# Kernel tuning notes

Hardware: AMD Instinct MI355X
Metric: run time of the kernel (lower is better)

Reference implementation:

```python
import jax, jax.numpy as jnp
import numpy as np

DT = 0.01
T, D_IN, D_STATE = 262144, 64, 128

def setup_inputs() -> dict:
    key = jax.random.key(0)
    k1, k2, k3, k4 = jax.random.split(key, 4)
    U = jax.random.normal(k1, (T, D_IN), dtype=jnp.float32)
    A_log = jax.random.normal(k2, (D_STATE,), dtype=jnp.float32) * 0.1 - 1.0
    B = jax.random.normal(k3, (D_STATE, D_IN), dtype=jnp.float32) * 0.1
    C = jax.random.normal(k4, (D_IN, D_STATE), dtype=jnp.float32) * 0.1
    Dm = jnp.zeros((D_IN, D_IN), dtype=jnp.float32)
    h0 = jnp.zeros((D_STATE,), dtype=jnp.float32)
    return {"U": U, "A_log": A_log, "B": B, "C": C, "D": Dm, "h0": h0}

def reference(U, A_log, B, C, D, h0):
    # Discretized diagonal transition: A_disc = exp(A_log * dt)
    A_d = jnp.exp(A_log * DT)  # (d_state,)
    Bu = U @ B.T               # (T, d_state), precompute all input injections
    Du = U @ D.T               # (T, d_input)

    def step(h, bu):
        h_new = A_d * h + bu
        return h_new, h_new

    h_final, H = jax.lax.scan(step, h0, Bu)  # H: (T, d_state)
    Y = H @ C.T + Du                          # (T, d_input)
    return Y, h_final
```

## Files before the change

### kernel.cpp

```cpp
#include <hip/hip_runtime.h>


#define TT   262144
#define DIN  64
#define DS   128
#define DTC  0.01f
#define L    128
#define NG   (TT / L)
#define SEGL 16
#define NSEG (NG / SEGL)

typedef short  s8v  __attribute__((ext_vector_type(8)));
typedef short  s4v  __attribute__((ext_vector_type(4)));
typedef float  f4v  __attribute__((ext_vector_type(4)));

__device__ __forceinline__ unsigned short f2bf(float f) {
    unsigned u = __float_as_uint(f);
    u += 0x7fffu + ((u >> 16) & 1u);
    return (unsigned short)(u >> 16);
}

__device__ __forceinline__ s8v pack8(float4 a, float4 b) {
    union { unsigned short u[8]; s8v v; } r;
    r.u[0] = f2bf(a.x); r.u[1] = f2bf(a.y); r.u[2] = f2bf(a.z); r.u[3] = f2bf(a.w);
    r.u[4] = f2bf(b.x); r.u[5] = f2bf(b.y); r.u[6] = f2bf(b.z); r.u[7] = f2bf(b.w);
    return r.v;
}

__device__ __forceinline__ s4v pack4(float x, float y, float z, float w) {
    union { unsigned short u[4]; s4v v; } r;
    r.u[0] = f2bf(x); r.u[1] = f2bf(y); r.u[2] = f2bf(z); r.u[3] = f2bf(w);
    return r.v;
}

__device__ __forceinline__ int gidx(int NCO, int rtile, int co, int mf) {
    return (((rtile * NCO + co) << 4) + (mf ^ (co & 15))) << 3;
}

__device__ __forceinline__ s8v ldfrag(const unsigned short* S, int NCO,
                                      int rtile, int kt, int q, int m) {
    return *(const s8v*)&S[gidx(NCO, rtile, kt * 4 + q, m)];
}

__device__ __forceinline__ void stage_U(const float* __restrict__ Ug,
                                        unsigned short* __restrict__ sA,
                                        int tid) {
    #pragma unroll
    for (int p = 0; p < 2; ++p) {
        int u  = tid + p * 512;
        int co = u & 7, m = (u >> 3) & 15, mt = u >> 7;
        const float4* gp = (const float4*)(Ug + (mt * 16 + m) * DIN + co * 8);
        *(s8v*)&sA[gidx(8, mt, co, m)] = pack8(gp[0], gp[1]);
    }
}

__device__ __forceinline__ s8v load_bfrag(const float* __restrict__ M,
                                          int row, int k0, int ld) {
    const float4* p = (const float4*)(M + row * ld + k0);
    return pack8(p[0], p[1]);
}

__global__ __launch_bounds__(512, 8) void ssm_k1(
    const float* __restrict__ U, const float* __restrict__ Alog,
    const float* __restrict__ B, float* __restrict__ agg,
    float* __restrict__ segAgg)
{
    __shared__ __align__(16) unsigned short sA[8192];
    const int g    = blockIdx.x;
    const int tid  = threadIdx.x;
    const int lane = tid & 63;
    const int w    = tid >> 6;
    const int q    = lane >> 4, m = lane & 15;
    const int s    = 16 * w + m;

    stage_U(U + (size_t)g * L * DIN, sA, tid);

    s8v Bf[2];
    #pragma unroll
    for (int ks = 0; ks < 2; ++ks)
        Bf[ks] = load_bfrag(B, s, ks * 32 + q * 8, DIN);

    const float cA = Alog[s] * DTC;
    __syncthreads();

    float ainv = __expf(-cA);
    float a16i = __expf(-16.f * cA);
    float wmt  = __expf(cA * (float)(127 - 4 * q));
    float wsum = 0.f;
    #pragma unroll
    for (int mt = 0; mt < 8; ++mt) {
        f4v acc = (f4v){0.f, 0.f, 0.f, 0.f};
        #pragma unroll
        for (int ks = 0; ks < 2; ++ks)
            acc = __builtin_amdgcn_mfma_f32_16x16x32_bf16(
                ldfrag(sA, 8, mt, ks, q, m), Bf[ks], acc, 0, 0, 0);
        float wr = wmt;
        #pragma unroll
        for (int r = 0; r < 4; ++r) {
            wsum = fmaf(wr, acc[r], wsum);
            wr *= ainv;
        }
        wmt *= a16i;
    }
    wsum += __shfl_xor(wsum, 16, 64);
    wsum += __shfl_xor(wsum, 32, 64);

    if (q == 0) {
        agg[(size_t)g * DS + s] = wsum;
        float wgt = __expf(cA * (float)(L * (SEGL - 1 - (g & (SEGL - 1)))));
        atomicAdd(&segAgg[(g >> 4) * DS + s], wsum * wgt);
    }
}

__global__ void ssm_k2(const float* __restrict__ Alog, const float* __restrict__ h0,
                       const float* __restrict__ segAgg, float* __restrict__ segCarry,
                       float* __restrict__ hfin)
{
    const int s = threadIdx.x;
    const float aSeg = __expf(Alog[s] * (DTC * L * SEGL));
    float c = h0[s];
    #pragma unroll 8
    for (int sg = 0; sg < NSEG; ++sg) {
        segCarry[sg * DS + s] = c;
        c = fmaf(aSeg, c, segAgg[sg * DS + s]);
    }
    hfin[s] = c;
}

__global__ __launch_bounds__(512, 6) void ssm_k3(
    const float* __restrict__ U, const float* __restrict__ Alog,
    const float* __restrict__ B, const float* __restrict__ C,
    const float* __restrict__ Dm, const float* __restrict__ agg,
    const float* __restrict__ segCarry, float* __restrict__ Y)
{
    __shared__ __align__(16) unsigned char smem[49152];
    unsigned short* sA = (unsigned short*)smem;
    unsigned short* sT = (unsigned short*)(smem + 16384);
    float*          sY = (float*)smem;
    __shared__ float sCA[DS];
    __shared__ float sDc[DS];

    const int g    = blockIdx.x;
    const int tid  = threadIdx.x;
    const int lane = tid & 63;
    const int w    = tid >> 6;
    const int q    = lane >> 4, m = lane & 15;

    s8v Bf[2];
    #pragma unroll
    for (int ks = 0; ks < 2; ++ks)
        Bf[ks] = load_bfrag(B, 16 * w + m, ks * 32 + q * 8, DIN);
    const float cA = Alog[16 * w + m] * DTC;

    stage_U(U + (size_t)g * L * DIN, sA, tid);

    if (tid < DS) {
        const float ca  = Alog[tid] * DTC;
        sCA[tid] = ca;
        const float caL = ca * (float)L;
        const float aL  = __expf(caL);
        const int   j   = g & (SEGL - 1);
        const int   gb  = g & ~(SEGL - 1);
        float c0 = segCarry[(g >> 4) * DS + tid] * __expf(caL * (float)j);
        float wt = 1.f;
        for (int c = j - 1; c >= 0; --c) {
            c0 = fmaf(wt, agg[(size_t)(gb + c) * DS + tid], c0);
            wt *= aL;
        }
        sDc[tid] = __expf(ca) * c0;
    }
    __syncthreads();

    {
        float ainv = __expf(-cA);
        float a16i = __expf(-16.f * cA);
        float fmt  = __expf(-cA * (float)(4 * q));
        #pragma unroll
        for (int mt = 0; mt < 8; ++mt) {
            f4v acc = (f4v){0.f, 0.f, 0.f, 0.f};
            #pragma unroll
            for (int ks = 0; ks < 2; ++ks)
                acc = __builtin_amdgcn_mfma_f32_16x16x32_bf16(
                    ldfrag(sA, 8, mt, ks, q, m), Bf[ks], acc, 0, 0, 0);
            float f0 = fmt, f1 = f0 * ainv, f2 = f1 * ainv, f3 = f2 * ainv;
            s4v pk = pack4(acc[0] * f0, acc[1] * f1, acc[2] * f2, acc[3] * f3);
            *(s4v*)&sT[gidx(16, w, mt * 2 + (q >> 1), m) + (q & 1) * 4] = pk;
            fmt *= a16i;
        }
    }
    __syncthreads();

    const int KBmax = w >> 1;
    const int thr   = m + 16 * (w & 1);
    s8v ones, part;
    {
        union { unsigned short u[8]; s8v v; } o, p;
        #pragma unroll
        for (int j = 0; j < 8; ++j) {
            o.u[j] = 0x3F80;
            p.u[j] = (q * 8 + j <= thr) ? 0x3F80 : 0;
        }
        ones = o.v; part = p.v;
    }
    const float tf = (float)(16 * w + m);
    s4v pk[8];
    #pragma unroll
    for (int grp = 0; grp < 2; ++grp) {
        f4v acc[4];
        #pragma unroll
        for (int i = 0; i < 4; ++i) acc[i] = (f4v){0.f, 0.f, 0.f, 0.f};
        for (int kb = 0; kb <= KBmax; ++kb) {
            s8v bfr = (kb < KBmax) ? ones : part;
            #pragma unroll
            for (int msl = 0; msl < 4; ++msl)
                acc[msl] = __builtin_amdgcn_mfma_f32_16x16x32_bf16(
                    ldfrag(sT, 16, grp * 4 + msl, kb, q, m), bfr, acc[msl], 0, 0, 0);
        }
        #pragma unroll
        for (int msl = 0; msl < 4; ++msl) {
            const int ms = grp * 4 + msl;
            const float4 cav = *(const float4*)&sCA[16 * ms + 4 * q];
            const float4 dcv = *(const float4*)&sDc[16 * ms + 4 * q];
            pk[grp * 4 + msl] = pack4(
                __expf(cav.x * tf) * (acc[msl][0] + dcv.x),
                __expf(cav.y * tf) * (acc[msl][1] + dcv.y),
                __expf(cav.z * tf) * (acc[msl][2] + dcv.z),
                __expf(cav.w * tf) * (acc[msl][3] + dcv.w));
        }
    }

    const int mi = w & 3, th = w >> 2;
    float4 craw[4][2], draw[2][2];
    #pragma unroll
    for (int ks = 0; ks < 4; ++ks) {
        const float4* p = (const float4*)(C + (16 * mi + m) * DS + ks * 32 + q * 8);
        craw[ks][0] = p[0]; craw[ks][1] = p[1];
    }
    #pragma unroll
    for (int ks = 0; ks < 2; ++ks) {
        const float4* p = (const float4*)(Dm + (16 * mi + m) * DIN + ks * 32 + q * 8);
        draw[ks][0] = p[0]; draw[ks][1] = p[1];
    }

    __syncthreads();
    #pragma unroll
    for (int ms = 0; ms < 8; ++ms)
        *(s4v*)&sT[gidx(16, w, ms * 2 + (q >> 1), m) + (q & 1) * 4] = pk[ms];
    __syncthreads();

    s8v Cf[4], Df[2];
    #pragma unroll
    for (int ks = 0; ks < 4; ++ks) Cf[ks] = pack8(craw[ks][0], craw[ks][1]);
    #pragma unroll
    for (int ks = 0; ks < 2; ++ks) Df[ks] = pack8(draw[ks][0], draw[ks][1]);

    f4v acc2[4];
    #pragma unroll
    for (int nn = 0; nn < 4; ++nn) {
        const int nt2 = th * 4 + nn;
        f4v a2 = (f4v){0.f, 0.f, 0.f, 0.f};
        #pragma unroll
        for (int ks = 0; ks < 4; ++ks)
            a2 = __builtin_amdgcn_mfma_f32_16x16x32_bf16(
                Cf[ks], ldfrag(sT, 16, nt2, ks, q, m), a2, 0, 0, 0);
        #pragma unroll
        for (int ks = 0; ks < 2; ++ks)
            a2 = __builtin_amdgcn_mfma_f32_16x16x32_bf16(
                Df[ks], ldfrag(sA, 8, nt2, ks, q, m), a2, 0, 0, 0);
        acc2[nn] = a2;
    }
    __syncthreads();

    #pragma unroll
    for (int nn = 0; nn < 4; ++nn) {
        const int t = 16 * (th * 4 + nn) + m;
        *(f4v*)&sY[t * 68 + 16 * mi + 4 * q] = acc2[nn];
    }
    __syncthreads();

    float* Yb = Y + (size_t)g * L * DIN;
    #pragma unroll
    for (int k = 0; k < 4; ++k) {
        const int f   = tid + 512 * k;
        const int row = f >> 4;
        const int col = (f & 15) << 2;
        *(float4*)(Yb + row * 64 + col) = *(const float4*)&sY[row * 68 + col];
    }
}

extern "C" void kernel_launch(void* const* d_in, const int* in_sizes, int n_in,
                              void* d_out, int out_size, void* d_ws, size_t ws_size,
                              hipStream_t stream)
{
    const float* U    = (const float*)d_in[0];
    const float* Alog = (const float*)d_in[1];
    const float* B    = (const float*)d_in[2];
    const float* C    = (const float*)d_in[3];
    const float* Dm   = (const float*)d_in[4];
    const float* h0   = (const float*)d_in[5];

    float* out  = (float*)d_out;
    float* Yp   = out;
    float* hfin = out + (size_t)TT * DIN;

    float* agg      = (float*)d_ws;
    float* segAgg   = agg + (size_t)NG * DS;
    float* segCarry = segAgg + (size_t)NSEG * DS;

    hipMemsetAsync(segAgg, 0, (size_t)NSEG * DS * sizeof(float), stream);
    ssm_k1<<<NG, 512, 0, stream>>>(U, Alog, B, agg, segAgg);
    ssm_k2<<<1, DS, 0, stream>>>(Alog, h0, segAgg, segCarry, hfin);
    ssm_k3<<<NG, 512, 0, stream>>>(U, Alog, B, C, Dm, agg, segCarry, Yp);
}
```

Before: 199.4 us.

## Process four chunks per block in ssm_k1 with double-buffered U prefetch

```diff
diff --git a/kernel.cpp b/kernel.cpp
--- a/kernel.cpp
+++ b/kernel.cpp
@@ -9,6 +9,7 @@
 #define NG   (TT / L)
 #define SEGL 16
 #define NSEG (NG / SEGL)
+#define CPB  4
 
 typedef short  s8v  __attribute__((ext_vector_type(8)));
 typedef short  s4v  __attribute__((ext_vector_type(4)));
@@ -54,61 +55,94 @@
     }
 }
 
+__device__ __forceinline__ void load_U_regs(const float* __restrict__ Ug,
+                                            int tid, float4 r[4]) {
+    #pragma unroll
+    for (int p = 0; p < 2; ++p) {
+        int u  = tid + p * 512;
+        int co = u & 7, m = (u >> 3) & 15, mt = u >> 7;
+        const float4* gp = (const float4*)(Ug + (mt * 16 + m) * DIN + co * 8);
+        r[2 * p]     = gp[0];
+        r[2 * p + 1] = gp[1];
+    }
+}
+
+__device__ __forceinline__ void write_U_lds(unsigned short* __restrict__ sA,
+                                            int tid, const float4 r[4]) {
+    #pragma unroll
+    for (int p = 0; p < 2; ++p) {
+        int u  = tid + p * 512;
+        int co = u & 7, m = (u >> 3) & 15, mt = u >> 7;
+        *(s8v*)&sA[gidx(8, mt, co, m)] = pack8(r[2 * p], r[2 * p + 1]);
+    }
+}
+
 __device__ __forceinline__ s8v load_bfrag(const float* __restrict__ M,
                                           int row, int k0, int ld) {
     const float4* p = (const float4*)(M + row * ld + k0);
     return pack8(p[0], p[1]);
 }
 
-__global__ __launch_bounds__(512, 8) void ssm_k1(
+__global__ __launch_bounds__(512, 4) void ssm_k1(
     const float* __restrict__ U, const float* __restrict__ Alog,
     const float* __restrict__ B, float* __restrict__ agg,
     float* __restrict__ segAgg)
 {
-    __shared__ __align__(16) unsigned short sA[8192];
-    const int g    = blockIdx.x;
+    __shared__ __align__(16) unsigned short sA[2][8192];
+    const int g0   = blockIdx.x * CPB;
     const int tid  = threadIdx.x;
     const int lane = tid & 63;
     const int w    = tid >> 6;
     const int q    = lane >> 4, m = lane & 15;
     const int s    = 16 * w + m;
 
-    stage_U(U + (size_t)g * L * DIN, sA, tid);
-
     s8v Bf[2];
     #pragma unroll
     for (int ks = 0; ks < 2; ++ks)
         Bf[ks] = load_bfrag(B, s, ks * 32 + q * 8, DIN);
-
-    const float cA = Alog[s] * DTC;
-    __syncthreads();
-
-    float ainv = __expf(-cA);
-    float a16i = __expf(-16.f * cA);
-    float wmt  = __expf(cA * (float)(127 - 4 * q));
-    float wsum = 0.f;
-    #pragma unroll
-    for (int mt = 0; mt < 8; ++mt) {
-        f4v acc = (f4v){0.f, 0.f, 0.f, 0.f};
-        #pragma unroll
-        for (int ks = 0; ks < 2; ++ks)
-            acc = __builtin_amdgcn_mfma_f32_16x16x32_bf16(
-                ldfrag(sA, 8, mt, ks, q, m), Bf[ks], acc, 0, 0, 0);
-        float wr = wmt;
-        #pragma unroll
-        for (int r = 0; r < 4; ++r) {
-            wsum = fmaf(wr, acc[r], wsum);
-            wr *= ainv;
-        }
-        wmt *= a16i;
-    }
-    wsum += __shfl_xor(wsum, 16, 64);
-    wsum += __shfl_xor(wsum, 32, 64);
-
-    if (q == 0) {
-        agg[(size_t)g * DS + s] = wsum;
-        float wgt = __expf(cA * (float)(L * (SEGL - 1 - (g & (SEGL - 1)))));
-        atomicAdd(&segAgg[(g >> 4) * DS + s], wsum * wgt);
+    const float cA   = Alog[s] * DTC;
+    const float ainv = __expf(-cA);
+    const float a16i = __expf(-16.f * cA);
+    const float wmt0 = __expf(cA * (float)(127 - 4 * q));
+    const float aSegStep = __expf(-cA * (float)L);
+    float wgt = __expf(cA * (float)(L * (SEGL - 1 - (g0 & (SEGL - 1)))));
+
+    float4 ureg[4];
+    load_U_regs(U + (size_t)g0 * L * DIN, tid, ureg);
+
+    for (int c = 0; c < CPB; ++c) {
+        const int g = g0 + c;
+        unsigned short* sAb = &sA[c & 1][0];
+        write_U_lds(sAb, tid, ureg);
+        if (c + 1 < CPB)
+            load_U_regs(U + (size_t)(g + 1) * L * DIN, tid, ureg);
+        __syncthreads();
+
+        float wmt  = wmt0;
+        float wsum = 0.f;
+        #pragma unroll
+        for (int mt = 0; mt < 8; ++mt) {
+            f4v acc = (f4v){0.f, 0.f, 0.f, 0.f};
+            #pragma unroll
+            for (int ks = 0; ks < 2; ++ks)
+                acc = __builtin_amdgcn_mfma_f32_16x16x32_bf16(
+                    ldfrag(sAb, 8, mt, ks, q, m), Bf[ks], acc, 0, 0, 0);
+            float wr = wmt;
+            #pragma unroll
+            for (int r = 0; r < 4; ++r) {
+                wsum = fmaf(wr, acc[r], wsum);
+                wr *= ainv;
+            }
+            wmt *= a16i;
+        }
+        wsum += __shfl_xor(wsum, 16, 64);
+        wsum += __shfl_xor(wsum, 32, 64);
+
+        if (q == 0) {
+            agg[(size_t)g * DS + s] = wsum;
+            atomicAdd(&segAgg[(g >> 4) * DS + s], wsum * wgt);
+        }
+        wgt *= aSegStep;
     }
 }
 
@@ -308,7 +342,7 @@
     float* segCarry = segAgg + (size_t)NSEG * DS;
 
     hipMemsetAsync(segAgg, 0, (size_t)NSEG * DS * sizeof(float), stream);
-    ssm_k1<<<NG, 512, 0, stream>>>(U, Alog, B, agg, segAgg);
+    ssm_k1<<<NG / CPB, 512, 0, stream>>>(U, Alog, B, agg, segAgg);
     ssm_k2<<<1, DS, 0, stream>>>(Alog, h0, segAgg, segCarry, hfin);
     ssm_k3<<<NG, 512, 0, stream>>>(U, Alog, B, C, Dm, agg, segCarry, Yp);
 }
```

Result: slower. 203.9 us (+2.3%).
